# Optimization experiments

Measured on AMD Instinct MI355X. Metric: run time of the kernel, lower is better.

The kernel has to match this reference:

```python
import jax, jax.numpy as jnp
import numpy as np

N = 100000   # num_nodes
E = 1000000  # num_edges
H = 64       # hidden_dim
M = 64       # msg_dim
C = 16       # num_classes


def setup_inputs() -> dict:
    key = jax.random.key(0)
    ks = jax.random.split(key, 16)
    s = 1.0 / np.sqrt(H)
    inp = {
        "features": jax.random.normal(ks[0], (N, H), jnp.float32),
        "src": jax.random.randint(ks[1], (E,), 0, N, dtype=jnp.int32),
        "dst": jax.random.randint(ks[2], (E,), 0, N, dtype=jnp.int32),
        "edge_types": jax.random.randint(ks[3], (E,), 0, 2, dtype=jnp.int32) == 1,
        # per-edge-type message linears (edge_matrix[0] for type==True, [1] for type==False)
        "W0": jax.random.uniform(ks[4], (M, H), jnp.float32, -s, s),
        "b0": jax.random.uniform(ks[5], (M,), jnp.float32, -s, s),
        "W1": jax.random.uniform(ks[6], (M, H), jnp.float32, -s, s),
        "b1": jax.random.uniform(ks[7], (M,), jnp.float32, -s, s),
        # GRU (single layer, single step): gates order [r, z, n] as in torch
        "W_ih": jax.random.uniform(ks[8], (3 * H, M), jnp.float32, -s, s),
        "W_hh": jax.random.uniform(ks[9], (3 * H, H), jnp.float32, -s, s),
        "b_ih": jax.random.uniform(ks[10], (3 * H,), jnp.float32, -s, s),
        "b_hh": jax.random.uniform(ks[11], (3 * H,), jnp.float32, -s, s),
        # output classifier
        "W_out": jax.random.uniform(ks[12], (C, H), jnp.float32, -s, s),
        "b_out": jax.random.uniform(ks[13], (C,), jnp.float32, -s, s),
    }
    return inp


def reference(features, src, dst, edge_types,
              W0, b0, W1, b1, W_ih, W_hh, b_ih, b_hh, W_out, b_out):
    # gather source-node features per edge: [E, H]
    x = features[src]
    # tiny per-edge-type linear; select by edge type
    m0 = x @ W0.T + b0            # type True  -> edge_matrix[0]
    m1 = x @ W1.T + b1            # type False -> edge_matrix[1]
    msg = jnp.where(edge_types[:, None], m0, m1)  # [E, M]
    # scatter-add messages into node buffer (zero-initialized accumulator)
    agg = jax.ops.segment_sum(msg, dst, num_segments=N)  # [N, M]
    # single GRU step: input=agg, hidden=features
    gi = agg @ W_ih.T + b_ih       # [N, 3H]
    gh = features @ W_hh.T + b_hh  # [N, 3H]
    i_r, i_z, i_n = jnp.split(gi, 3, axis=-1)
    h_r, h_z, h_n = jnp.split(gh, 3, axis=-1)
    r = jax.nn.sigmoid(i_r + h_r)
    z = jax.nn.sigmoid(i_z + h_z)
    n = jnp.tanh(i_n + r * h_n)
    h = (1.0 - z) * n + z * features  # [N, H]
    # output classifier
    return h @ W_out.T + b_out        # [N, C]
```

## Files before the change

### kernel.cpp

```cpp
#include <hip/hip_runtime.h>


typedef __bf16 bf16x8 __attribute__((ext_vector_type(8)));
typedef float  f32x4  __attribute__((ext_vector_type(4)));
typedef int    i32x4  __attribute__((ext_vector_type(4)));

#define MFMA16 __builtin_amdgcn_mfma_f32_16x16x32_bf16
#define NN   100000
#define EE   1000000
#define BB   782
#define NPB  128
#define ECAP 1600
#define DCAP 48
#define CSTRD 49
#define NB   245
#define NW   33792

__device__ __forceinline__ float sigmoidf_(float x) {
    return 1.0f / (1.0f + __expf(-x));
}

__device__ __forceinline__ bf16x8 ldw(const __bf16* w, int e) {
    int bo = e * 2;
    bo ^= ((bo >> 7) & 7) << 4;
    return *(const bf16x8*)((const char*)w + bo);
}

__global__ __launch_bounds__(256) void k_init(const unsigned char* __restrict__ et,
                                              const float* __restrict__ feat,
                                              const float* __restrict__ w0,
                                              const float* __restrict__ w1,
                                              const float* __restrict__ wih,
                                              const float* __restrict__ whh,
                                              const float* __restrict__ wout,
                                              __bf16* __restrict__ featb,
                                              __bf16* __restrict__ wb,
                                              int* __restrict__ flag) {
    int b = blockIdx.x, tid = threadIdx.x;
    if (b == 0) {
        __shared__ int sdet[4];
        const i32x4* p = (const i32x4*)et + tid * 16;
        unsigned acc = 0;
#pragma unroll
        for (int j = 0; j < 16; j++) {
            i32x4 w = p[j];
            acc |= (unsigned)(w[0] | w[1] | w[2] | w[3]) & 0xffffff00u;
        }
        unsigned long long m = __ballot(acc != 0);
        if ((tid & 63) == 0) sdet[tid >> 6] = (m != 0ULL);
        __syncthreads();
        if (tid == 0) *flag = sdet[0] | sdet[1] | sdet[2] | sdet[3];
        return;
    }
    if (b < 133) {
        int i = (b - 1) * 256 + tid;
        float v;
        if      (i < 4096)  v = w0[i];
        else if (i < 8192)  v = w1[i - 4096];
        else if (i < 20480) v = wih[i - 8192];
        else if (i < 32768) v = whh[i - 20480];
        else                v = wout[i - 32768];
        wb[i] = (__bf16)v;
        return;
    }
    long i = ((long)(b - 133) * 256 + tid) * 4;
    if (i >= (long)NN * 64) return;
    f32x4 v = *(const f32x4*)(feat + i);
    union { __bf16 e[4]; unsigned long long u; } o;
#pragma unroll
    for (int j = 0; j < 4; j++) o.e[j] = (__bf16)v[j];
    *(unsigned long long*)(featb + i) = o.u;
}

__global__ __launch_bounds__(512) void k_s1(const int* __restrict__ dst,
                                            int* __restrict__ hist) {
    __shared__ int cnt[BB];
    int blk = blockIdx.x, tid = threadIdx.x;
    for (int i = tid; i < BB; i += 512) cnt[i] = 0;
    __syncthreads();
    long e0 = (long)blk * 4096 + tid * 8;
    if (e0 < EE) {
        i32x4 d0 = *(const i32x4*)(dst + e0);
        i32x4 d1 = *(const i32x4*)(dst + e0 + 4);
#pragma unroll
        for (int j = 0; j < 4; j++) atomicAdd(&cnt[d0[j] >> 7], 1);
#pragma unroll
        for (int j = 0; j < 4; j++) atomicAdd(&cnt[d1[j] >> 7], 1);
    }
    __syncthreads();
    for (int i = tid; i < BB; i += 512) hist[blk * BB + i] = cnt[i];
}

__global__ __launch_bounds__(256) void k_s2(const int* __restrict__ hist,
                                            int* __restrict__ blockBase,
                                            int* __restrict__ bucketCnt) {
    int b = blockIdx.x * 4 + (threadIdx.x >> 6);
    int lane = threadIdx.x & 63;
    if (b >= BB) return;
    int carry = 0;
    for (int c = 0; c < 4; c++) {
        int blk = c * 64 + lane;
        int v = (blk < NB) ? hist[blk * BB + b] : 0;
        int x = v;
#pragma unroll
        for (int off = 1; off < 64; off <<= 1) {
            int y = __shfl_up(x, off, 64);
            if (lane >= off) x += y;
        }
        if (blk < NB) blockBase[blk * BB + b] = x - v + carry;
        carry += __shfl(x, 63, 64);
    }
    if (lane == 0) bucketCnt[b] = carry;
}

__global__ __launch_bounds__(512) void k_s3(const int* __restrict__ src,
                                            const int* __restrict__ dst,
                                            const unsigned char* __restrict__ etype,
                                            const int* __restrict__ flag,
                                            const int* __restrict__ blockBase,
                                            int* __restrict__ region) {
    __shared__ int cur[BB];
    int blk = blockIdx.x, tid = threadIdx.x;
    for (int i = tid; i < BB; i += 512) cur[i] = blockBase[blk * BB + i];
    __syncthreads();
    long e0 = (long)blk * 4096 + tid * 8;
    if (e0 >= EE) return;
    i32x4 s0 = *(const i32x4*)(src + e0);
    i32x4 s1 = *(const i32x4*)(src + e0 + 4);
    i32x4 d0 = *(const i32x4*)(dst + e0);
    i32x4 d1 = *(const i32x4*)(dst + e0 + 4);
    int t[8];
    if (*flag) {
        unsigned long long w = *(const unsigned long long*)(etype + e0);
#pragma unroll
        for (int j = 0; j < 8; j++) t[j] = (int)((w >> (8 * j)) & 0xff);
    } else {
        i32x4 w0 = *(const i32x4*)((const int*)etype + e0);
        i32x4 w1 = *(const i32x4*)((const int*)etype + e0 + 4);
#pragma unroll
        for (int j = 0; j < 4; j++) { t[j] = w0[j]; t[4 + j] = w1[j]; }
    }
    int dd[8] = {d0[0], d0[1], d0[2], d0[3], d1[0], d1[1], d1[2], d1[3]};
    int ss[8] = {s0[0], s0[1], s0[2], s0[3], s1[0], s1[1], s1[2], s1[3]};
#pragma unroll
    for (int j = 0; j < 8; j++) {
        int b  = dd[j] >> 7;
        int nl = dd[j] & 127;
        int r  = atomicAdd(&cur[b], 1);
        if (r < ECAP)
            region[b * ECAP + r] = (nl << 18) | ((t[j] ? 1 : 0) << 17) | ss[j];
    }
}

__global__ __launch_bounds__(512) void k_g(const __bf16* __restrict__ featb,
                                           const int* __restrict__ region,
                                           const int* __restrict__ bucketCnt,
                                           __bf16* __restrict__ s1b,
                                           __bf16* __restrict__ s0b,
                                           int* __restrict__ cc) {
    __shared__ int ncnt[NPB];
    __shared__ int csr[NPB * CSTRD];
    int b = blockIdx.x, tid = threadIdx.x;
    int cntE = min(bucketCnt[b], ECAP);
    if (tid < NPB) ncnt[tid] = 0;
    __syncthreads();
    const int* reg = region + b * ECAP;
    for (int i = tid; i < cntE; i += 512) {
        int rec = reg[i];
        int nl = rec >> 18;
        int r = atomicAdd(&ncnt[nl], 1);
        if (r < DCAP) csr[nl * CSTRD + r] = rec & 0x3ffff;
    }
    __syncthreads();

    int lane = tid & 63, wave = tid >> 6;
    int L = lane & 15, q = lane >> 4;
    int nl = wave * 16 + L;
    int n = b * NPB + nl;
    int cnt = (n < NN) ? min(ncnt[nl], DCAP) : 0;
    const int* eb = &csr[nl * CSTRD];

    float sA[16], s1[16];
#pragma unroll
    for (int j = 0; j < 16; j++) { sA[j] = 0.f; s1[j] = 0.f; }
    int c1 = 0;
    int i = 0;
    for (; i + 2 <= cnt; i += 2) {
        int ea = eb[i], ebn = eb[i + 1];
        const __bf16* rowa = featb + (long)(ea & 0x1ffff) * 64;
        const __bf16* rowb = featb + (long)(ebn & 0x1ffff) * 64;
        bf16x8 a0 = *(const bf16x8*)(rowa + q * 8);
        bf16x8 a1 = *(const bf16x8*)(rowa + 32 + q * 8);
        bf16x8 b0v = *(const bf16x8*)(rowb + q * 8);
        bf16x8 b1v = *(const bf16x8*)(rowb + 32 + q * 8);
        int ta = (ea >> 17) & 1, tb = (ebn >> 17) & 1;
        c1 += ta + tb;
        float fa = (float)ta, fb = (float)tb;
#pragma unroll
        for (int j = 0; j < 8; j++) {
            float va = (float)a0[j], wa = (float)a1[j];
            float vb = (float)b0v[j], wb2 = (float)b1v[j];
            sA[j]     += va + vb;
            sA[8 + j] += wa + wb2;
            s1[j]     += fa * va + fb * vb;
            s1[8 + j] += fa * wa + fb * wb2;
        }
    }
    if (i < cnt) {
        int ea = eb[i];
        const __bf16* rowa = featb + (long)(ea & 0x1ffff) * 64;
        bf16x8 a0 = *(const bf16x8*)(rowa + q * 8);
        bf16x8 a1 = *(const bf16x8*)(rowa + 32 + q * 8);
        int ta = (ea >> 17) & 1;
        c1 += ta;
        float fa = (float)ta;
#pragma unroll
        for (int j = 0; j < 8; j++) {
            float va = (float)a0[j], wa = (float)a1[j];
            sA[j] += va;          sA[8 + j] += wa;
            s1[j] += fa * va;     s1[8 + j] += fa * wa;
        }
    }
    if (n >= NN) return;
    union { bf16x8 v; __bf16 e[8]; } u;
#pragma unroll
    for (int ch = 0; ch < 2; ch++) {
#pragma unroll
        for (int j = 0; j < 8; j++) u.e[j] = (__bf16)s1[ch * 8 + j];
        *(bf16x8*)(s1b + (long)n * 64 + ch * 32 + q * 8) = u.v;
#pragma unroll
        for (int j = 0; j < 8; j++) u.e[j] = (__bf16)(sA[ch * 8 + j] - s1[ch * 8 + j]);
        *(bf16x8*)(s0b + (long)n * 64 + ch * 32 + q * 8) = u.v;
    }
    if (q == 0) cc[n] = cnt | (c1 << 16);
}

__global__ __launch_bounds__(512, 2) void k_mm(const __bf16* __restrict__ s1b,
                                               const __bf16* __restrict__ s0b,
                                               const __bf16* __restrict__ featb,
                                               const float* __restrict__ feat,
                                               const int* __restrict__ cc,
                                               const __bf16* __restrict__ wb,
                                               const float* __restrict__ b0,
                                               const float* __restrict__ b1,
                                               const float* __restrict__ bih,
                                               const float* __restrict__ bhh,
                                               const float* __restrict__ bout,
                                               float* __restrict__ out) {
    __shared__ __align__(16) __bf16 wlds[NW];
    __shared__ __align__(16) char smem[8][4352];
    int tid = threadIdx.x, lane = tid & 63, wave = tid >> 6;
    int L = lane & 15, q = lane >> 4;
    int n0 = blockIdx.x * NPB + wave * 16;

    bf16x8 AS1[2], AS0[2], Aft[2];
    float fvv[4][4], fc1[4], fc0[4];
    if (n0 < NN) {
        const __bf16* r1 = s1b + (long)(n0 + L) * 64;
        const __bf16* r0 = s0b + (long)(n0 + L) * 64;
        const __bf16* fr = featb + (long)(n0 + L) * 64;
        AS1[0] = *(const bf16x8*)(r1 + q * 8);  AS1[1] = *(const bf16x8*)(r1 + 32 + q * 8);
        AS0[0] = *(const bf16x8*)(r0 + q * 8);  AS0[1] = *(const bf16x8*)(r0 + 32 + q * 8);
        Aft[0] = *(const bf16x8*)(fr + q * 8);  Aft[1] = *(const bf16x8*)(fr + 32 + q * 8);
#pragma unroll
        for (int nb = 0; nb < 4; nb++)
#pragma unroll
            for (int r = 0; r < 4; r++)
                fvv[nb][r] = feat[(long)(n0 + q * 4 + r) * 64 + nb * 16 + L];
#pragma unroll
        for (int r = 0; r < 4; r++) {
            int v = cc[n0 + q * 4 + r];
            int c1 = v >> 16, ct = v & 0xffff;
            fc1[r] = (float)c1; fc0[r] = (float)(ct - c1);
        }
    }

    for (int k = tid * 8; k < NW; k += 512 * 8) {
        bf16x8 v = *(const bf16x8*)(wb + k);
        int bo = k * 2;
        int so = bo ^ (((bo >> 7) & 7) << 4);
        *(bf16x8*)((char*)wlds + so) = v;
    }
    __syncthreads();
    if (n0 >= NN) return;

    float*  sT = (float*)smem[wave];
    __bf16* sH = (__bf16*)smem[wave];
    f32x4 zz = {0.f, 0.f, 0.f, 0.f};

#pragma unroll
    for (int nb = 0; nb < 4; nb++) {
        f32x4 acc = zz;
#pragma unroll
        for (int ch = 0; ch < 2; ch++) {
            int off = (nb * 16 + L) * 64 + ch * 32 + q * 8;
            acc = MFMA16(AS1[ch], ldw(wlds, off), acc, 0, 0, 0);
            acc = MFMA16(AS0[ch], ldw(wlds, 4096 + off), acc, 0, 0, 0);
        }
        float bs0 = b0[nb * 16 + L], bs1 = b1[nb * 16 + L];
#pragma unroll
        for (int r = 0; r < 4; r++)
            sT[(q * 4 + r) * 68 + nb * 16 + L] = acc[r] + fc1[r] * bs0 + fc0[r] * bs1;
    }

    bf16x8 Aag[2];
#pragma unroll
    for (int ch = 0; ch < 2; ch++) {
        union { bf16x8 v; __bf16 e[8]; } u;
#pragma unroll
        for (int j2 = 0; j2 < 8; j2++) u.e[j2] = (__bf16)sT[L * 68 + ch * 32 + q * 8 + j2];
        Aag[ch] = u.v;
    }

#pragma unroll
    for (int nb = 0; nb < 4; nb++) {
        int row = nb * 16 + L;
        f32x4 aR = zz, aZ = zz, aIN = zz, aHN = zz;
#pragma unroll
        for (int ch = 0; ch < 2; ch++) {
            int ko = ch * 32 + q * 8;
            aR  = MFMA16(Aag[ch], ldw(wlds, 8192  + row * 64 + ko), aR, 0, 0, 0);
            aR  = MFMA16(Aft[ch], ldw(wlds, 20480 + row * 64 + ko), aR, 0, 0, 0);
            aZ  = MFMA16(Aag[ch], ldw(wlds, 8192  + (64 + row) * 64 + ko), aZ, 0, 0, 0);
            aZ  = MFMA16(Aft[ch], ldw(wlds, 20480 + (64 + row) * 64 + ko), aZ, 0, 0, 0);
            aIN = MFMA16(Aag[ch], ldw(wlds, 8192  + (128 + row) * 64 + ko), aIN, 0, 0, 0);
            aHN = MFMA16(Aft[ch], ldw(wlds, 20480 + (128 + row) * 64 + ko), aHN, 0, 0, 0);
        }
        int h = row;
        float br  = bih[h] + bhh[h];
        float bz  = bih[64 + h] + bhh[64 + h];
        float bin = bih[128 + h];
        float bhn = bhh[128 + h];
#pragma unroll
        for (int r = 0; r < 4; r++) {
            float rv = sigmoidf_(aR[r] + br);
            float zv = sigmoidf_(aZ[r] + bz);
            float nv = tanhf(aIN[r] + bin + rv * (aHN[r] + bhn));
            float fv = fvv[nb][r];
            sH[(q * 4 + r) * 80 + h] = (__bf16)((1.0f - zv) * nv + zv * fv);
        }
    }

    bf16x8 Ah0 = *(const bf16x8*)&sH[L * 80 + q * 8];
    bf16x8 Ah1 = *(const bf16x8*)&sH[L * 80 + 32 + q * 8];
    bf16x8 Bo0 = ldw(wlds, 32768 + L * 64 + q * 8);
    bf16x8 Bo1 = ldw(wlds, 32768 + L * 64 + 32 + q * 8);
    f32x4 o = zz;
    o = MFMA16(Ah0, Bo0, o, 0, 0, 0);
    o = MFMA16(Ah1, Bo1, o, 0, 0, 0);
    float bo = bout[L];
#pragma unroll
    for (int r = 0; r < 4; r++)
        out[(long)(n0 + q * 4 + r) * 16 + L] = o[r] + bo;
}

extern "C" void kernel_launch(void* const* d_in, const int* in_sizes, int n_in,
                              void* d_out, int out_size, void* d_ws, size_t ws_size,
                              hipStream_t stream) {
    const float* features = (const float*)d_in[0];
    const int*   src      = (const int*)d_in[1];
    const int*   dst      = (const int*)d_in[2];
    const unsigned char* etype = (const unsigned char*)d_in[3];
    const float* W0   = (const float*)d_in[4];
    const float* b0   = (const float*)d_in[5];
    const float* W1   = (const float*)d_in[6];
    const float* b1   = (const float*)d_in[7];
    const float* Wih  = (const float*)d_in[8];
    const float* Whh  = (const float*)d_in[9];
    const float* bih  = (const float*)d_in[10];
    const float* bhh  = (const float*)d_in[11];
    const float* Wout = (const float*)d_in[12];
    const float* bout = (const float*)d_in[13];
    float* out = (float*)d_out;

    char* ws = (char*)d_ws;
    size_t off = 0;
    __bf16* featb     = (__bf16*)(ws + off); off += (size_t)NN * 64 * 2;
    int*    region    = (int*)(ws + off);    off += (size_t)BB * ECAP * 4;
    int*    hist      = (int*)(ws + off);    off += (size_t)NB * BB * 4;
    int*    blockBase = (int*)(ws + off);    off += (size_t)NB * BB * 4;
    int*    bucketCnt = (int*)(ws + off);    off += (size_t)BB * 4;
    int*    cc        = (int*)(ws + off);    off += (size_t)NN * 4;
    __bf16* s1b       = (__bf16*)(ws + off); off += (size_t)NN * 64 * 2;
    __bf16* s0b       = (__bf16*)(ws + off); off += (size_t)NN * 64 * 2;
    __bf16* wb        = (__bf16*)(ws + off); off += 33792 * 2;
    int*    flag      = (int*)(ws + off);

    k_init<<<6383, 256, 0, stream>>>(etype, features, W0, W1, Wih, Whh, Wout,
                                     featb, wb, flag);
    k_s1<<<NB, 512, 0, stream>>>(dst, hist);
    k_s2<<<(BB + 3) / 4, 256, 0, stream>>>(hist, blockBase, bucketCnt);
    k_s3<<<NB, 512, 0, stream>>>(src, dst, etype, flag, blockBase, region);
    k_g<<<BB, 512, 0, stream>>>(featb, region, bucketCnt, s1b, s0b, cc);
    k_mm<<<BB, 512, 0, stream>>>(s1b, s0b, featb, features, cc, wb,
                                 b0, b1, bih, bhh, bout, out);
}
```

Before: 187.3 us.

## Merge histogram into init kernel and shrink k_mm LDS for higher occupancy

Folds the destination-bucket histogram pass into the init kernel as extra blocks, which removes one kernel launch. In the final kernel, only the GRU weights stay in LDS. The small message and output weights are read straight from global memory, and the per-wave scratch is reduced to a bf16 tile, so LDS use drops and launch bounds allow 4 blocks per CU. The message accumulator is now rounded to bf16 in LDS before the GRU instead of being kept in fp32. The uncached weight loads from global or L2 could add latency.

```diff
diff --git a/kernel.cpp b/kernel.cpp
--- a/kernel.cpp
+++ b/kernel.cpp
@@ -14,7 +14,7 @@
 #define DCAP 48
 #define CSTRD 49
 #define NB   245
-#define NW   33792
+#define NWL  24576
 
 __device__ __forceinline__ float sigmoidf_(float x) {
     return 1.0f / (1.0f + __expf(-x));
@@ -28,6 +28,7 @@
 
 __global__ __launch_bounds__(256) void k_init(const unsigned char* __restrict__ et,
                                               const float* __restrict__ feat,
+                                              const int* __restrict__ dst,
                                               const float* __restrict__ w0,
                                               const float* __restrict__ w1,
                                               const float* __restrict__ wih,
@@ -35,6 +36,7 @@
                                               const float* __restrict__ wout,
                                               __bf16* __restrict__ featb,
                                               __bf16* __restrict__ wb,
+                                              int* __restrict__ hist,
                                               int* __restrict__ flag) {
     int b = blockIdx.x, tid = threadIdx.x;
     if (b == 0) {
@@ -63,6 +65,28 @@
         wb[i] = (__bf16)v;
         return;
     }
+    if (b >= 6383) {
+        __shared__ int cnt[BB];
+        int hb = b - 6383;
+        for (int i = tid; i < BB; i += 256) cnt[i] = 0;
+        __syncthreads();
+        long e0 = (long)hb * 4096 + tid * 16;
+#pragma unroll
+        for (int g = 0; g < 2; g++) {
+            long e = e0 + g * 8;
+            if (e < EE) {
+                i32x4 d0 = *(const i32x4*)(dst + e);
+                i32x4 d1 = *(const i32x4*)(dst + e + 4);
+#pragma unroll
+                for (int j = 0; j < 4; j++) atomicAdd(&cnt[d0[j] >> 7], 1);
+#pragma unroll
+                for (int j = 0; j < 4; j++) atomicAdd(&cnt[d1[j] >> 7], 1);
+            }
+        }
+        __syncthreads();
+        for (int i = tid; i < BB; i += 256) hist[hb * BB + i] = cnt[i];
+        return;
+    }
     long i = ((long)(b - 133) * 256 + tid) * 4;
     if (i >= (long)NN * 64) return;
     f32x4 v = *(const f32x4*)(feat + i);
@@ -70,25 +94,6 @@
 #pragma unroll
     for (int j = 0; j < 4; j++) o.e[j] = (__bf16)v[j];
     *(unsigned long long*)(featb + i) = o.u;
-}
-
-__global__ __launch_bounds__(512) void k_s1(const int* __restrict__ dst,
-                                            int* __restrict__ hist) {
-    __shared__ int cnt[BB];
-    int blk = blockIdx.x, tid = threadIdx.x;
-    for (int i = tid; i < BB; i += 512) cnt[i] = 0;
-    __syncthreads();
-    long e0 = (long)blk * 4096 + tid * 8;
-    if (e0 < EE) {
-        i32x4 d0 = *(const i32x4*)(dst + e0);
-        i32x4 d1 = *(const i32x4*)(dst + e0 + 4);
-#pragma unroll
-        for (int j = 0; j < 4; j++) atomicAdd(&cnt[d0[j] >> 7], 1);
-#pragma unroll
-        for (int j = 0; j < 4; j++) atomicAdd(&cnt[d1[j] >> 7], 1);
-    }
-    __syncthreads();
-    for (int i = tid; i < BB; i += 512) hist[blk * BB + i] = cnt[i];
 }
 
 __global__ __launch_bounds__(256) void k_s2(const int* __restrict__ hist,
@@ -235,7 +240,7 @@
     if (q == 0) cc[n] = cnt | (c1 << 16);
 }
 
-__global__ __launch_bounds__(512, 2) void k_mm(const __bf16* __restrict__ s1b,
+__global__ __launch_bounds__(512, 4) void k_mm(const __bf16* __restrict__ s1b,
                                                const __bf16* __restrict__ s0b,
                                                const __bf16* __restrict__ featb,
                                                const float* __restrict__ feat,
@@ -247,8 +252,8 @@
                                                const float* __restrict__ bhh,
                                                const float* __restrict__ bout,
                                                float* __restrict__ out) {
-    __shared__ __align__(16) __bf16 wlds[NW];
-    __shared__ __align__(16) char smem[8][4352];
+    __shared__ __align__(16) __bf16 wlds[NWL];
+    __shared__ __align__(16) __bf16 sHall[8][16 * 80];
     int tid = threadIdx.x, lane = tid & 63, wave = tid >> 6;
     int L = lane & 15, q = lane >> 4;
     int n0 = blockIdx.x * NPB + wave * 16;
@@ -267,16 +272,17 @@
 #pragma unroll
             for (int r = 0; r < 4; r++)
                 fvv[nb][r] = feat[(long)(n0 + q * 4 + r) * 64 + nb * 16 + L];
+        i32x4 cv = *(const i32x4*)(cc + n0 + q * 4);
 #pragma unroll
         for (int r = 0; r < 4; r++) {
-            int v = cc[n0 + q * 4 + r];
-            int c1 = v >> 16, ct = v & 0xffff;
+            int c1 = cv[r] >> 16, ct = cv[r] & 0xffff;
             fc1[r] = (float)c1; fc0[r] = (float)(ct - c1);
         }
     }
 
-    for (int k = tid * 8; k < NW; k += 512 * 8) {
-        bf16x8 v = *(const bf16x8*)(wb + k);
+    const __bf16* wsrc = wb + 8192;
+    for (int k = tid * 8; k < NWL; k += 512 * 8) {
+        bf16x8 v = *(const bf16x8*)(wsrc + k);
         int bo = k * 2;
         int so = bo ^ (((bo >> 7) & 7) << 4);
         *(bf16x8*)((char*)wlds + so) = v;
@@ -284,8 +290,8 @@
     __syncthreads();
     if (n0 >= NN) return;
 
-    float*  sT = (float*)smem[wave];
-    __bf16* sH = (__bf16*)smem[wave];
+    __bf16* sH = sHall[wave];
+    const __bf16* w0b = wb, * w1b = wb + 4096, * woutb = wb + 32768;
     f32x4 zz = {0.f, 0.f, 0.f, 0.f};
 
 #pragma unroll
@@ -294,23 +300,20 @@
 #pragma unroll
         for (int ch = 0; ch < 2; ch++) {
             int off = (nb * 16 + L) * 64 + ch * 32 + q * 8;
-            acc = MFMA16(AS1[ch], ldw(wlds, off), acc, 0, 0, 0);
-            acc = MFMA16(AS0[ch], ldw(wlds, 4096 + off), acc, 0, 0, 0);
+            acc = MFMA16(AS1[ch], *(const bf16x8*)(w0b + off), acc, 0, 0, 0);
+            acc = MFMA16(AS0[ch], *(const bf16x8*)(w1b + off), acc, 0, 0, 0);
         }
         float bs0 = b0[nb * 16 + L], bs1 = b1[nb * 16 + L];
 #pragma unroll
         for (int r = 0; r < 4; r++)
-            sT[(q * 4 + r) * 68 + nb * 16 + L] = acc[r] + fc1[r] * bs0 + fc0[r] * bs1;
+            sH[(q * 4 + r) * 80 + nb * 16 + L] =
+                (__bf16)(acc[r] + fc1[r] * bs0 + fc0[r] * bs1);
     }
 
     bf16x8 Aag[2];
 #pragma unroll
-    for (int ch = 0; ch < 2; ch++) {
-        union { bf16x8 v; __bf16 e[8]; } u;
-#pragma unroll
-        for (int j2 = 0; j2 < 8; j2++) u.e[j2] = (__bf16)sT[L * 68 + ch * 32 + q * 8 + j2];
-        Aag[ch] = u.v;
-    }
+    for (int ch = 0; ch < 2; ch++)
+        Aag[ch] = *(const bf16x8*)&sH[L * 80 + ch * 32 + q * 8];
 
 #pragma unroll
     for (int nb = 0; nb < 4; nb++) {
@@ -319,12 +322,12 @@
 #pragma unroll
         for (int ch = 0; ch < 2; ch++) {
             int ko = ch * 32 + q * 8;
-            aR  = MFMA16(Aag[ch], ldw(wlds, 8192  + row * 64 + ko), aR, 0, 0, 0);
-            aR  = MFMA16(Aft[ch], ldw(wlds, 20480 + row * 64 + ko), aR, 0, 0, 0);
-            aZ  = MFMA16(Aag[ch], ldw(wlds, 8192  + (64 + row) * 64 + ko), aZ, 0, 0, 0);
-            aZ  = MFMA16(Aft[ch], ldw(wlds, 20480 + (64 + row) * 64 + ko), aZ, 0, 0, 0);
-            aIN = MFMA16(Aag[ch], ldw(wlds, 8192  + (128 + row) * 64 + ko), aIN, 0, 0, 0);
-            aHN = MFMA16(Aft[ch], ldw(wlds, 20480 + (128 + row) * 64 + ko), aHN, 0, 0, 0);
+            aR  = MFMA16(Aag[ch], ldw(wlds, row * 64 + ko), aR, 0, 0, 0);
+            aR  = MFMA16(Aft[ch], ldw(wlds, 12288 + row * 64 + ko), aR, 0, 0, 0);
+            aZ  = MFMA16(Aag[ch], ldw(wlds, (64 + row) * 64 + ko), aZ, 0, 0, 0);
+            aZ  = MFMA16(Aft[ch], ldw(wlds, 12288 + (64 + row) * 64 + ko), aZ, 0, 0, 0);
+            aIN = MFMA16(Aag[ch], ldw(wlds, (128 + row) * 64 + ko), aIN, 0, 0, 0);
+            aHN = MFMA16(Aft[ch], ldw(wlds, 12288 + (128 + row) * 64 + ko), aHN, 0, 0, 0);
         }
         int h = row;
         float br  = bih[h] + bhh[h];
@@ -343,8 +346,8 @@
 
     bf16x8 Ah0 = *(const bf16x8*)&sH[L * 80 + q * 8];
     bf16x8 Ah1 = *(const bf16x8*)&sH[L * 80 + 32 + q * 8];
-    bf16x8 Bo0 = ldw(wlds, 32768 + L * 64 + q * 8);
-    bf16x8 Bo1 = ldw(wlds, 32768 + L * 64 + 32 + q * 8);
+    bf16x8 Bo0 = *(const bf16x8*)(woutb + L * 64 + q * 8);
+    bf16x8 Bo1 = *(const bf16x8*)(woutb + L * 64 + 32 + q * 8);
     f32x4 o = zz;
     o = MFMA16(Ah0, Bo0, o, 0, 0, 0);
     o = MFMA16(Ah1, Bo1, o, 0, 0, 0);
@@ -386,9 +389,8 @@
     __bf16* wb        = (__bf16*)(ws + off); off += 33792 * 2;
     int*    flag      = (int*)(ws + off);
 
-    k_init<<<6383, 256, 0, stream>>>(etype, features, W0, W1, Wih, Whh, Wout,
-                                     featb, wb, flag);
-    k_s1<<<NB, 512, 0, stream>>>(dst, hist);
+    k_init<<<6628, 256, 0, stream>>>(etype, features, dst, W0, W1, Wih, Whh,
+                                     Wout, featb, wb, hist, flag);
     k_s2<<<(BB + 3) / 4, 256, 0, stream>>>(hist, blockBase, bucketCnt);
     k_s3<<<NB, 512, 0, stream>>>(src, dst, etype, flag, blockBase, region);
     k_g<<<BB, 512, 0, stream>>>(featb, region, bucketCnt, s1b, s0b, cc);
```

After: 185.3 us. Within noise of the previous version (-1.1%).
